# Performance work log

Hardware: AMD Instinct MI355X
Metric: run time of the kernel (lower is better)

Reference implementation:

```python
import jax, jax.numpy as jnp
import numpy as np
import math

D_QKV = 64


def setup_inputs() -> dict:
    key = jax.random.key(0)
    ks = jax.random.split(key, 6)
    b, l, d_model, n_head, d_qkv = 2, 2048, 1024, 16, D_QKV
    return {
        "x": jax.random.normal(ks[0], (b, l, d_model), dtype=jnp.float32),
        "w_q": jax.random.normal(ks[1], (n_head, d_model, d_qkv), dtype=jnp.float32) * (2.0 / (d_model + d_qkv)) ** 0.5,
        "w_k": jax.random.normal(ks[2], (n_head, d_model, d_qkv), dtype=jnp.float32) * (2.0 / (d_model + d_qkv)) ** 0.5,
        "w_v": jax.random.normal(ks[3], (n_head, d_model, d_qkv), dtype=jnp.float32) * (2.0 / (d_model + d_qkv)) ** 0.5,
        "w_o": jax.random.normal(ks[4], (n_head, d_qkv, d_model), dtype=jnp.float32) * (2.0 / (d_model + d_qkv)) ** 0.5,
        "mask": jnp.zeros((b, 1, 1, l), dtype=bool),  # True = masked (padding)
    }


def reference(x, w_q, w_k, w_v, w_o, mask):
    # x: [b, l, m]; w_{q,k,v}: [n, m, d]; w_o: [n, d, m]; mask broadcastable to [b, n, l, l]
    q = jnp.einsum("blm,nmd->bnld", x, w_q)
    k = jnp.einsum("blm,nmd->bnld", x, w_k)
    v = jnp.einsum("blm,nmd->bnld", x, w_v)
    scores = jnp.einsum("bnld,bnkd->bnlk", q, k) / math.sqrt(D_QKV)
    scores = jnp.where(mask, jnp.float32(-1e9), scores)
    attn = jax.nn.softmax(scores, axis=-1)  # dropout is identity (p=0 / eval)
    ctx = jnp.einsum("bnlk,bnkd->bnld", attn, v)
    # per-head output projection then sum over heads: V.matmul(w_o).sum(dim=1)
    return jnp.einsum("bnld,ndm->blm", ctx, w_o)
```

## Files before the change

### kernel.cpp

```cpp
#include <hip/hip_runtime.h>
#include <stdint.h>

using bf16x8  = __attribute__((ext_vector_type(8))) short;
using f32x4   = __attribute__((ext_vector_type(4))) float;
using f32x16  = __attribute__((ext_vector_type(16))) float;
using ushort8 = __attribute__((ext_vector_type(8))) unsigned short;
using ushort4v= __attribute__((ext_vector_type(4))) unsigned short;
using uint2v  = __attribute__((ext_vector_type(2))) unsigned int;
using f32x4v  = __attribute__((ext_vector_type(4))) float;

typedef __attribute__((address_space(1))) const unsigned int* gas_ptr;
typedef __attribute__((address_space(3))) unsigned int*       las_ptr;

__device__ __forceinline__ void gload_lds16(const unsigned short* g, unsigned short* l) {
    __builtin_amdgcn_global_load_lds((gas_ptr)(const void*)g, (las_ptr)(void*)l, 16, 0, 0);
}

__device__ __forceinline__ unsigned short f2bf(float f) {
    union { float f; uint32_t u; } x; x.f = f;
    uint32_t u = x.u;
    uint32_t r = u + 0x7fffu + ((u >> 16) & 1u);
    return (unsigned short)(r >> 16);
}
__device__ __forceinline__ float bf2f(unsigned short u) {
    union { uint32_t u; float f; } x; x.u = ((uint32_t)u) << 16;
    return x.f;
}

__device__ __forceinline__ f32x4 mfma16(bf16x8 a, bf16x8 b, f32x4 c) {
    return __builtin_amdgcn_mfma_f32_16x16x32_bf16(a, b, c, 0, 0, 0);
}
__device__ __forceinline__ f32x16 mfma32(bf16x8 a, bf16x8 b, f32x16 c) {
    return __builtin_amdgcn_mfma_f32_32x32x16_bf16(a, b, c, 0, 0, 0);
}

__device__ __forceinline__ unsigned int cvtpk_bf16(float lo, float hi) {
    unsigned int r;
    asm("v_cvt_pk_bf16_f32 %0, %1, %2" : "=v"(r) : "v"(lo), "v"(hi));
    return r;
}
__device__ __forceinline__ void plswap(unsigned int& a, unsigned int& b) {
    asm("v_permlane32_swap_b32 %0, %1" : "+v"(a), "+v"(b));
}
__device__ __forceinline__ float m3(float a, float b, float c) {
    return fmaxf(fmaxf(a, b), c);
}


__global__ void prep_kernel(const float* __restrict__ x,
                            const float* __restrict__ wq, const float* __restrict__ wk,
                            const float* __restrict__ wv, const float* __restrict__ wo,
                            unsigned short* __restrict__ xb, unsigned short* __restrict__ wpT,
                            unsigned short* __restrict__ woT)
{
    __shared__ float tile[64][65];
    const int bid = blockIdx.x;
    const int tid = threadIdx.x;

    if (bid < 4096) {
        int i = bid * 256 + tid;
        f32x4v v = ((const f32x4v*)x)[i];
        ushort4v o;
        o[0] = f2bf(v[0]); o[1] = f2bf(v[1]); o[2] = f2bf(v[2]); o[3] = f2bf(v[3]);
        ((ushort4v*)xb)[i] = o;
    } else if (bid < 4864) {
        const int b2 = bid - 4096;
        const int mm = b2 >> 4;
        const int s = mm >> 4, hh = mm & 15;
        const float* src = ((s == 0) ? wq : (s == 1) ? wk : wv) + (size_t)hh * 1024 * 64;
        const int k0 = (b2 & 15) * 64;
        const int c = tid & 63, rg = tid >> 6;
#pragma unroll
        for (int i = 0; i < 16; ++i) {
            int r = rg * 16 + i;
            tile[r][c] = src[(size_t)(k0 + r) * 64 + c];
        }
        __syncthreads();
        unsigned short* dst = wpT + ((size_t)s * 1024 + hh * 64) * 1024 + k0;
        const int kc = tid & 63, dg = tid >> 6;
#pragma unroll
        for (int i = 0; i < 16; ++i) {
            int d = dg * 16 + i;
            dst[(size_t)d * 1024 + kc] = f2bf(tile[kc][d]);
        }
    } else {
        const int b3 = bid - 4864;
        const int r0 = (b3 >> 4) * 64;
        const int c0 = (b3 & 15) * 64;
        const int c = tid & 63, rg = tid >> 6;
#pragma unroll
        for (int i = 0; i < 16; ++i) {
            int r = rg * 16 + i;
            tile[r][c] = wo[(size_t)(r0 + r) * 1024 + c0 + c];
        }
        __syncthreads();
        const int kc = tid & 63, mg = tid >> 6;
#pragma unroll
        for (int i = 0; i < 16; ++i) {
            int m = mg * 16 + i;
            woT[(size_t)(c0 + m) * 1024 + r0 + kc] = f2bf(tile[kc][m]);
        }
    }
}


template<int MODE, int BN>
__global__ __launch_bounds__(256) void gemm_bt(
    const unsigned short* __restrict__ A,
    const unsigned short* __restrict__ BT,
    float* __restrict__ Cf,
    unsigned short* __restrict__ Q,
    unsigned short* __restrict__ Kq,
    unsigned short* __restrict__ V,
    int M, int N, int K)
{
    constexpr int NF = BN / 32;
    __shared__ unsigned short As[128 * 64];
    __shared__ unsigned short Bs[BN * 64];
    const int tid  = threadIdx.x;
    const int lane = tid & 63;
    const int wave = tid >> 6;
    const int wm = wave >> 1, wn = wave & 1;
    const int l15 = lane & 15, l4 = lane >> 4;
    const int row0 = blockIdx.y * 128;
    const int col0 = blockIdx.x * BN;

    f32x4 acc[4][NF];
#pragma unroll
    for (int i = 0; i < 4; ++i)
#pragma unroll
        for (int j = 0; j < NF; ++j) acc[i][j] = (f32x4){0.f, 0.f, 0.f, 0.f};

    for (int k0 = 0; k0 < K; k0 += 64) {
        __syncthreads();
#pragma unroll
        for (int it = 0; it < 4; ++it) {
            int cb = (it * 4 + wave) * 64;
            int c  = cb + lane;
            int r  = c >> 3, c8 = c & 7;
            int sc8 = c8 ^ (r & 7);
            gload_lds16(&A[(size_t)(row0 + r) * K + k0 + sc8 * 8], &As[cb * 8]);
        }
#pragma unroll
        for (int it = 0; it < NF; ++it) {
            int cb = (it * 4 + wave) * 64;
            int c  = cb + lane;
            int r  = c >> 3, c8 = c & 7;
            int sc8 = c8 ^ (r & 7);
            gload_lds16(&BT[(size_t)(col0 + r) * K + k0 + sc8 * 8], &Bs[cb * 8]);
        }
        __syncthreads();
#pragma unroll
        for (int kk = 0; kk < 2; ++kk) {
            bf16x8 af[4], bfr[NF];
#pragma unroll
            for (int m = 0; m < 4; ++m) {
                int r   = wm * 64 + m * 16 + l15;
                int blk = (kk * 4 + l4) ^ (r & 7);
                af[m] = *(const bf16x8*)&As[r * 64 + blk * 8];
            }
#pragma unroll
            for (int n = 0; n < NF; ++n) {
                int r   = wn * (BN / 2) + n * 16 + l15;
                int blk = (kk * 4 + l4) ^ (r & 7);
                bfr[n] = *(const bf16x8*)&Bs[r * 64 + blk * 8];
            }
#pragma unroll
            for (int m = 0; m < 4; ++m)
#pragma unroll
                for (int n = 0; n < NF; ++n)
                    acc[m][n] = mfma16(af[m], bfr[n], acc[m][n]);
        }
    }

#pragma unroll
    for (int m = 0; m < 4; ++m) {
        int gr0 = row0 + wm * 64 + m * 16 + l4 * 4;
#pragma unroll
        for (int n = 0; n < NF; ++n) {
            int gc = col0 + wn * (BN / 2) + n * 16 + l15;
            if (MODE == 0) {
                int s = gc >> 10, rem = gc & 1023;
                int hh = rem >> 6, dd = rem & 63;
                int bb = gr0 >> 11, ll = gr0 & 2047;
                if (s == 2) {
                    ushort4v o;
#pragma unroll
                    for (int r = 0; r < 4; ++r) o[r] = f2bf(acc[m][n][r]);
                    *(ushort4v*)&V[(((size_t)bb * 16 + hh) * 64 + dd) * 2048 + ll] = o;
                } else {
                    unsigned short* dst = (s == 0) ? Q : Kq;
#pragma unroll
                    for (int r = 0; r < 4; ++r)
                        dst[(((size_t)bb * 16 + hh) * 2048 + ll + r) * 64 + dd] = f2bf(acc[m][n][r]);
                }
            } else {
#pragma unroll
                for (int r = 0; r < 4; ++r)
                    Cf[(size_t)(gr0 + r) * N + gc] = acc[m][n][r];
            }
        }
    }
}


__global__ __launch_bounds__(256, 4) void attn_kernel(
    const unsigned short* __restrict__ qb,
    const unsigned short* __restrict__ kb,
    const unsigned short* __restrict__ vtb,
    const unsigned char* __restrict__ mask,
    unsigned short* __restrict__ part0,
    unsigned short* __restrict__ part1,
    float* __restrict__ ml)
{
    const int lg = blockIdx.x;
    int u = ((lg & 7) << 7) | (lg >> 3);
    int bh = u >> 5, sub = u & 31;
    const int qt = sub >> 1, half = sub & 1;
    const int b = bh >> 4;
    const int t0 = half * 16;
    const int NT = 16;

    const int tid  = threadIdx.x;
    const int lane = tid & 63, wave = tid >> 6;
    const int l31  = lane & 31, hi = lane >> 5;

    __shared__ unsigned short smem[16384];

    const size_t hoff = (size_t)bh * 131072;
    const unsigned short* qh  = qb  + hoff;
    const unsigned short* kh  = kb  + hoff;
    const unsigned short* vth = vtb + hoff;
    const unsigned char*  mb  = mask + (size_t)b * 2048;

    unsigned long long mball;
    {
        const uint2v* mp = (const uint2v*)mb;
        uint2v a0 = mp[lane * 4 + 0], a1 = mp[lane * 4 + 1];
        uint2v a2 = mp[lane * 4 + 2], a3 = mp[lane * 4 + 3];
        unsigned int any = a0[0] | a0[1] | a1[0] | a1[1] | a2[0] | a2[1] | a3[0] | a3[1];
        mball = __ballot(any != 0u);
    }

    const int qrow = qt * 128 + wave * 32 + l31;
    bf16x8 qf[4];
#pragma unroll
    for (int ki = 0; ki < 4; ++ki)
        qf[ki] = *(const bf16x8*)&qh[(size_t)qrow * 64 + ki * 16 + hi * 8];

    const f32x16 zf = {0,0,0,0,0,0,0,0,0,0,0,0,0,0,0,0};
    bf16x8 ones;
#pragma unroll
    for (int j = 0; j < 8; ++j) ones[j] = (short)0x3F80;

    f32x16 accA = {0,0,0,0,0,0,0,0,0,0,0,0,0,0,0,0};
    f32x16 accB = {0,0,0,0,0,0,0,0,0,0,0,0,0,0,0,0};
    f32x16 accL = {0,0,0,0,0,0,0,0,0,0,0,0,0,0,0,0};
    float m_r = -1e30f;
    const float SC  = 0.18033688011112042f;
    const float THR = 44.3614195558365f;

#define STAGE(KB, VB, KV0) do {                                                          \
        _Pragma("unroll")                                                                \
        for (int it_ = 0; it_ < 2; ++it_) {                                              \
            int c_ = it_ * 256 + tid;                                                    \
            int r_ = c_ >> 3, c8_ = c_ & 7;                                              \
            int sc8_ = c8_ ^ (r_ & 7);                                                   \
            gload_lds16(&kh[(size_t)((KV0) + r_) * 64 + sc8_ * 8],                       \
                        &(KB)[(it_ * 256 + wave * 64) * 8]);                             \
            gload_lds16(&vth[(size_t)r_ * 2048 + (KV0) + sc8_ * 8],                      \
                        &(VB)[(it_ * 256 + wave * 64) * 8]);                             \
        }                                                                                \
    } while (0)

    STAGE(smem, smem + 8192, t0 * 64);

    for (int t = t0; t < t0 + NT; ++t) {
        const int kv0 = t * 64;
        unsigned short* Kb = smem + ((t - t0) & 1) * 4096;
        unsigned short* Vb = smem + 8192 + ((t - t0) & 1) * 4096;
        __syncthreads();
        if (t + 1 < t0 + NT) {
            unsigned short* Kn = smem + ((t + 1 - t0) & 1) * 4096;
            unsigned short* Vn = smem + 8192 + ((t + 1 - t0) & 1) * 4096;
            STAGE(Kn, Vn, kv0 + 64);
        }

        f32x16 s0, s1;
        __builtin_amdgcn_s_setprio(1);
        {
            int c0 = (hi ^ (l31 & 7)) * 8;
            bf16x8 a0 = *(const bf16x8*)&Kb[l31 * 64 + c0];
            bf16x8 a1 = *(const bf16x8*)&Kb[(32 + l31) * 64 + c0];
            s0 = mfma32(a0, qf[0], zf);
            s1 = mfma32(a1, qf[0], zf);
        }
#pragma unroll
        for (int ki = 1; ki < 4; ++ki) {
            int c0 = ((ki * 2 + hi) ^ (l31 & 7)) * 8;
            bf16x8 a0 = *(const bf16x8*)&Kb[l31 * 64 + c0];
            bf16x8 a1 = *(const bf16x8*)&Kb[(32 + l31) * 64 + c0];
            s0 = mfma32(a0, qf[ki], s0);
            s1 = mfma32(a1, qf[ki], s1);
        }
        __builtin_amdgcn_s_setprio(0);

        if ((mball >> ((t & 31) * 2)) & 3ull) {
#pragma unroll
            for (int r = 0; r < 16; ++r) {
                int keyl = (r & 3) + 8 * (r >> 2) + 4 * hi;
                if (mb[kv0 + keyl])      s0[r] = -1e30f;
                if (mb[kv0 + 32 + keyl]) s1[r] = -1e30f;
            }
        }

        float mx;
        {
            float a0 = m3(s0[0],  s0[1],  s0[2]);
            float a1 = m3(s0[3],  s0[4],  s0[5]);
            float a2 = m3(s0[6],  s0[7],  s0[8]);
            float a3 = m3(s0[9],  s0[10], s0[11]);
            float a4 = m3(s0[12], s0[13], s0[14]);
            float b0 = m3(s1[0],  s1[1],  s1[2]);
            float b1 = m3(s1[3],  s1[4],  s1[5]);
            float b2 = m3(s1[6],  s1[7],  s1[8]);
            float b3 = m3(s1[9],  s1[10], s1[11]);
            float b4 = m3(s1[12], s1[13], s1[14]);
            float c0 = m3(a0, a1, s0[15]);
            float c1 = m3(a2, a3, a4);
            float c2 = m3(b0, b1, s1[15]);
            float c3 = m3(b2, b3, b4);
            mx = fmaxf(m3(c0, c1, c2), c3);
        }
        mx = fmaxf(mx, __shfl_xor(mx, 32));
        if (__any(mx > m_r + THR)) {
            float mn  = fmaxf(m_r, mx);
            float scl = __builtin_amdgcn_exp2f((m_r - mn) * SC);
            m_r = mn;
            accL[0] *= scl;
#pragma unroll
            for (int i = 0; i < 16; ++i) { accA[i] *= scl; accB[i] *= scl; }
        }
        const float nmc = -m_r * SC;
#pragma unroll
        for (int i = 0; i < 16; ++i) {
            s0[i] = __builtin_amdgcn_exp2f(__builtin_fmaf(s0[i], SC, nmc));
            s1[i] = __builtin_amdgcn_exp2f(__builtin_fmaf(s1[i], SC, nmc));
        }

        bf16x8 pf[4];
        {
            union { unsigned int u[4]; bf16x8 v; } f;
            unsigned int w0 = cvtpk_bf16(s0[0],  s0[1]),  w1 = cvtpk_bf16(s0[2],  s0[3]);
            unsigned int w2 = cvtpk_bf16(s0[4],  s0[5]),  w3 = cvtpk_bf16(s0[6],  s0[7]);
            unsigned int w4 = cvtpk_bf16(s0[8],  s0[9]),  w5 = cvtpk_bf16(s0[10], s0[11]);
            unsigned int w6 = cvtpk_bf16(s0[12], s0[13]), w7 = cvtpk_bf16(s0[14], s0[15]);
            plswap(w0, w2); plswap(w1, w3); plswap(w4, w6); plswap(w5, w7);
            f.u[0] = w0; f.u[1] = w1; f.u[2] = w2; f.u[3] = w3; pf[0] = f.v;
            f.u[0] = w4; f.u[1] = w5; f.u[2] = w6; f.u[3] = w7; pf[1] = f.v;
            unsigned int x0 = cvtpk_bf16(s1[0],  s1[1]),  x1 = cvtpk_bf16(s1[2],  s1[3]);
            unsigned int x2 = cvtpk_bf16(s1[4],  s1[5]),  x3 = cvtpk_bf16(s1[6],  s1[7]);
            unsigned int x4 = cvtpk_bf16(s1[8],  s1[9]),  x5 = cvtpk_bf16(s1[10], s1[11]);
            unsigned int x6 = cvtpk_bf16(s1[12], s1[13]), x7 = cvtpk_bf16(s1[14], s1[15]);
            plswap(x0, x2); plswap(x1, x3); plswap(x4, x6); plswap(x5, x7);
            f.u[0] = x0; f.u[1] = x1; f.u[2] = x2; f.u[3] = x3; pf[2] = f.v;
            f.u[0] = x4; f.u[1] = x5; f.u[2] = x6; f.u[3] = x7; pf[3] = f.v;
        }

        __builtin_amdgcn_s_setprio(1);
#pragma unroll
        for (int ks = 0; ks < 4; ++ks) {
            int c0 = ((ks * 2 + hi) ^ (l31 & 7)) * 8;
            bf16x8 vA = *(const bf16x8*)&Vb[l31 * 64 + c0];
            bf16x8 vB = *(const bf16x8*)&Vb[(32 + l31) * 64 + c0];
            accA = mfma32(vA, pf[ks], accA);
            accB = mfma32(vB, pf[ks], accB);
            accL = mfma32(ones, pf[ks], accL);
        }
        __builtin_amdgcn_s_setprio(0);
    }
#undef STAGE

    __syncthreads();
    const int qloc = wave * 32 + l31;
#pragma unroll
    for (int r = 0; r < 16; ++r) {
        int dA = (r & 3) + 8 * (r >> 2) + 4 * hi;
        smem[qloc * 64 + (dA ^ ((qloc & 7) * 8))]        = f2bf(accA[r]);
        smem[qloc * 64 + ((32 + dA) ^ ((qloc & 7) * 8))] = f2bf(accB[r]);
    }
    if (hi == 0) {
        size_t mrow = ((size_t)half * 32 + bh) * 2048 + qt * 128 + qloc;
        *(float2*)&ml[mrow * 2] = make_float2(m_r, accL[0]);
    }
    __syncthreads();
    unsigned short* pdst = half ? part1 : part0;
    const size_t prow0 = (size_t)bh * 2048 + qt * 128;
#pragma unroll
    for (int it = 0; it < 4; ++it) {
        int idx = tid + it * 256;
        int q = idx >> 3, c = idx & 7;
        ushort8 vv = *(const ushort8*)&smem[q * 64 + ((c * 8) ^ ((q & 7) * 8))];
        *(ushort8*)&pdst[(prow0 + q) * 64 + c * 8] = vv;
    }
}


__global__ void combine_kernel(const unsigned short* __restrict__ part0,
                               const unsigned short* __restrict__ part1,
                               const float* __restrict__ ml,
                               unsigned short* __restrict__ ctxb)
{
    const float SC = 0.18033688011112042f;
    int gid = blockIdx.x * 256 + threadIdx.x;
    int row = gid >> 3, c = gid & 7;
    ushort8 v0 = *(const ushort8*)&part0[(size_t)row * 64 + c * 8];
    ushort8 v1 = *(const ushort8*)&part1[(size_t)row * 64 + c * 8];
    float2 a = *(const float2*)&ml[(size_t)row * 2];
    float2 d = *(const float2*)&ml[(size_t)(65536 + row) * 2];
    float m  = fmaxf(a.x, d.x);
    float w0 = __builtin_amdgcn_exp2f((a.x - m) * SC);
    float w1 = __builtin_amdgcn_exp2f((d.x - m) * SC);
    float li = 1.0f / (a.y * w0 + d.y * w1);
    ushort8 o;
#pragma unroll
    for (int j = 0; j < 8; ++j)
        o[j] = f2bf((bf2f(v0[j]) * w0 + bf2f(v1[j]) * w1) * li);
    int bh = row >> 11, ql = row & 2047;
    int bb = bh >> 4, hh = bh & 15;
    *(ushort8*)&ctxb[((size_t)(bb * 2048 + ql)) * 1024 + hh * 64 + c * 8] = o;
}


extern "C" void kernel_launch(void* const* d_in, const int* in_sizes, int n_in,
                              void* d_out, int out_size, void* d_ws, size_t ws_size,
                              hipStream_t stream)
{
    const float* x  = (const float*)d_in[0];
    const float* wq = (const float*)d_in[1];
    const float* wk = (const float*)d_in[2];
    const float* wv = (const float*)d_in[3];
    const float* wo = (const float*)d_in[4];
    const unsigned char* mask = (const unsigned char*)d_in[5];
    float* out = (float*)d_out;

    char* ws = (char*)d_ws;
    unsigned short* xb   = (unsigned short*)(ws);
    unsigned short* wpT  = (unsigned short*)(ws + 8388608);
    unsigned short* woT  = (unsigned short*)(ws + 14680064);
    unsigned short* qb   = (unsigned short*)(ws + 16777216);
    unsigned short* kb   = (unsigned short*)(ws + 25165824);
    unsigned short* vtb  = (unsigned short*)(ws + 33554432);
    unsigned short* ctxb = (unsigned short*)(ws + 41943040);
    unsigned short* part0 = (unsigned short*)d_out;
    unsigned short* part1 = (unsigned short*)d_out + 4194304;
    float*          mlb   = (float*)wpT;

    prep_kernel<<<5120, 256, 0, stream>>>(x, wq, wk, wv, wo, xb, wpT, woT);

    gemm_bt<0,128><<<dim3(24, 32), 256, 0, stream>>>(xb, wpT, nullptr, qb, kb, vtb, 4096, 3072, 1024);

    attn_kernel<<<1024, 256, 0, stream>>>(qb, kb, vtb, mask, part0, part1, mlb);
    combine_kernel<<<2048, 256, 0, stream>>>(part0, part1, mlb, ctxb);

    gemm_bt<1,64><<<dim3(16, 32), 256, 0, stream>>>(ctxb, woT, out, nullptr, nullptr, nullptr, 4096, 1024, 1024);
}
```

Baseline: 123.4 us.

## Drop split-KV attention and combine kernel; normalize context in-kernel

Each attention block now processes the full key/value sequence for its 128-query tile instead of half, normalizes by the running row sum, and writes bf16 context directly to the head-interleaved layout. This removes the separate combine kernel launch and the partial output and max/sum round trip through memory. In exchange the attention grid halves to 512 blocks with twice the loop length, reducing parallelism and occupancy across the GPU.

Measured after the change: 118.4 us (median of 2 runs). 4.0% less time.

```diff
diff --git a/kernel.cpp b/kernel.cpp
--- a/kernel.cpp
+++ b/kernel.cpp
@@ -209,17 +209,13 @@
     const unsigned short* __restrict__ kb,
     const unsigned short* __restrict__ vtb,
     const unsigned char* __restrict__ mask,
-    unsigned short* __restrict__ part0,
-    unsigned short* __restrict__ part1,
-    float* __restrict__ ml)
+    unsigned short* __restrict__ ctxb)
 {
     const int lg = blockIdx.x;
-    int u = ((lg & 7) << 7) | (lg >> 3);
-    int bh = u >> 5, sub = u & 31;
-    const int qt = sub >> 1, half = sub & 1;
+    int u = ((lg & 7) << 6) | (lg >> 3);
+    const int qt = u & 15, bh = u >> 4;
     const int b = bh >> 4;
-    const int t0 = half * 16;
-    const int NT = 16;
+    const int NT = 32;
 
     const int tid  = threadIdx.x;
     const int lane = tid & 63, wave = tid >> 6;
@@ -273,16 +269,16 @@
         }                                                                                \
     } while (0)
 
-    STAGE(smem, smem + 8192, t0 * 64);
-
-    for (int t = t0; t < t0 + NT; ++t) {
+    STAGE(smem, smem + 8192, 0);
+
+    for (int t = 0; t < NT; ++t) {
         const int kv0 = t * 64;
-        unsigned short* Kb = smem + ((t - t0) & 1) * 4096;
-        unsigned short* Vb = smem + 8192 + ((t - t0) & 1) * 4096;
+        unsigned short* Kb = smem + (t & 1) * 4096;
+        unsigned short* Vb = smem + 8192 + (t & 1) * 4096;
         __syncthreads();
-        if (t + 1 < t0 + NT) {
-            unsigned short* Kn = smem + ((t + 1 - t0) & 1) * 4096;
-            unsigned short* Vn = smem + 8192 + ((t + 1 - t0) & 1) * 4096;
+        if (t + 1 < NT) {
+            unsigned short* Kn = smem + ((t + 1) & 1) * 4096;
+            unsigned short* Vn = smem + 8192 + ((t + 1) & 1) * 4096;
             STAGE(Kn, Vn, kv0 + 64);
         }
 
@@ -382,53 +378,23 @@
 #undef STAGE
 
     __syncthreads();
+    const float inv = 1.0f / accL[0];
     const int qloc = wave * 32 + l31;
 #pragma unroll
     for (int r = 0; r < 16; ++r) {
         int dA = (r & 3) + 8 * (r >> 2) + 4 * hi;
-        smem[qloc * 64 + (dA ^ ((qloc & 7) * 8))]        = f2bf(accA[r]);
-        smem[qloc * 64 + ((32 + dA) ^ ((qloc & 7) * 8))] = f2bf(accB[r]);
-    }
-    if (hi == 0) {
-        size_t mrow = ((size_t)half * 32 + bh) * 2048 + qt * 128 + qloc;
-        *(float2*)&ml[mrow * 2] = make_float2(m_r, accL[0]);
+        smem[qloc * 64 + (dA ^ ((qloc & 7) * 8))]        = f2bf(accA[r] * inv);
+        smem[qloc * 64 + ((32 + dA) ^ ((qloc & 7) * 8))] = f2bf(accB[r] * inv);
     }
     __syncthreads();
-    unsigned short* pdst = half ? part1 : part0;
-    const size_t prow0 = (size_t)bh * 2048 + qt * 128;
+    const int h = bh & 15;
 #pragma unroll
     for (int it = 0; it < 4; ++it) {
         int idx = tid + it * 256;
         int q = idx >> 3, c = idx & 7;
         ushort8 vv = *(const ushort8*)&smem[q * 64 + ((c * 8) ^ ((q & 7) * 8))];
-        *(ushort8*)&pdst[(prow0 + q) * 64 + c * 8] = vv;
-    }
-}
-
-
-__global__ void combine_kernel(const unsigned short* __restrict__ part0,
-                               const unsigned short* __restrict__ part1,
-                               const float* __restrict__ ml,
-                               unsigned short* __restrict__ ctxb)
-{
-    const float SC = 0.18033688011112042f;
-    int gid = blockIdx.x * 256 + threadIdx.x;
-    int row = gid >> 3, c = gid & 7;
-    ushort8 v0 = *(const ushort8*)&part0[(size_t)row * 64 + c * 8];
-    ushort8 v1 = *(const ushort8*)&part1[(size_t)row * 64 + c * 8];
-    float2 a = *(const float2*)&ml[(size_t)row * 2];
-    float2 d = *(const float2*)&ml[(size_t)(65536 + row) * 2];
-    float m  = fmaxf(a.x, d.x);
-    float w0 = __builtin_amdgcn_exp2f((a.x - m) * SC);
-    float w1 = __builtin_amdgcn_exp2f((d.x - m) * SC);
-    float li = 1.0f / (a.y * w0 + d.y * w1);
-    ushort8 o;
-#pragma unroll
-    for (int j = 0; j < 8; ++j)
-        o[j] = f2bf((bf2f(v0[j]) * w0 + bf2f(v1[j]) * w1) * li);
-    int bh = row >> 11, ql = row & 2047;
-    int bb = bh >> 4, hh = bh & 15;
-    *(ushort8*)&ctxb[((size_t)(bb * 2048 + ql)) * 1024 + hh * 64 + c * 8] = o;
+        *(ushort8*)&ctxb[((size_t)(b * 2048 + qt * 128 + q)) * 1024 + h * 64 + c * 8] = vv;
+    }
 }
 
 
@@ -452,16 +418,12 @@
     unsigned short* kb   = (unsigned short*)(ws + 25165824);
     unsigned short* vtb  = (unsigned short*)(ws + 33554432);
     unsigned short* ctxb = (unsigned short*)(ws + 41943040);
-    unsigned short* part0 = (unsigned short*)d_out;
-    unsigned short* part1 = (unsigned short*)d_out + 4194304;
-    float*          mlb   = (float*)wpT;
 
     prep_kernel<<<5120, 256, 0, stream>>>(x, wq, wk, wv, wo, xb, wpT, woT);
 
     gemm_bt<0,128><<<dim3(24, 32), 256, 0, stream>>>(xb, wpT, nullptr, qb, kb, vtb, 4096, 3072, 1024);
 
-    attn_kernel<<<1024, 256, 0, stream>>>(qb, kb, vtb, mask, part0, part1, mlb);
-    combine_kernel<<<2048, 256, 0, stream>>>(part0, part1, mlb, ctxb);
+    attn_kernel<<<512, 256, 0, stream>>>(qb, kb, vtb, mask, ctxb);
 
     gemm_bt<1,64><<<dim3(16, 32), 256, 0, stream>>>(ctxb, woT, out, nullptr, nullptr, nullptr, 4096, 1024, 1024);
 }
```
